# Optimization experiments

Hardware: AMD Instinct MI355X
Metric: run time of the kernel (lower is better)

## Reference

```python
import jax, jax.numpy as jnp
import numpy as np

H = 1024

def setup_inputs() -> dict:
    key = jax.random.key(0)
    ks = jax.random.split(key, 7)
    B, S = 64, 2048
    decoder_hidden = jax.random.normal(ks[0], (B, H), dtype=jnp.float32)
    encoder_outputs = jax.random.normal(ks[1], (B, S, H), dtype=jnp.float32)
    sc = 1.0 / np.sqrt(H)
    W1_w = jax.random.normal(ks[2], (H, H), dtype=jnp.float32) * sc
    W1_b = jax.random.normal(ks[3], (H,), dtype=jnp.float32) * sc
    W2_w = jax.random.normal(ks[4], (H, H), dtype=jnp.float32) * sc
    W2_b = jax.random.normal(ks[5], (H,), dtype=jnp.float32) * sc
    v_w = jax.random.normal(ks[6], (H,), dtype=jnp.float32) * sc
    return {"decoder_hidden": decoder_hidden, "encoder_outputs": encoder_outputs,
            "W1_w": W1_w, "W1_b": W1_b, "W2_w": W2_w, "W2_b": W2_b, "v_w": v_w}

def reference(decoder_hidden, encoder_outputs, W1_w, W1_b, W2_w, W2_b, v_w):
    # enc proj: [B,S,H] @ [H,H] ; dec proj: [B,H] @ [H,H], broadcast over S
    enc_proj = jnp.einsum('bsh,hk->bsk', encoder_outputs, W1_w) + W1_b
    dec_proj = decoder_hidden @ W2_w + W2_b  # [B,H]
    e = jnp.tanh(enc_proj + dec_proj[:, None, :])  # [B,S,H]
    scores = jnp.einsum('bsh,h->bs', e, v_w)  # [B,S]
    attn_weights = jax.nn.softmax(scores, axis=1)
    context = jnp.einsum('bs,bsh->bh', attn_weights, encoder_outputs)
    return (context, attn_weights)
```

## Files before the change

### kernel.cpp

```cpp
#include <hip/hip_runtime.h>
#include <hip/hip_bf16.h>
#include <hip/hip_fp16.h>

#define HDIM 1024
#define BATCH 64
#define SEQ 2048
#define MTOT (BATCH*SEQ)
#define BM 128
#define BN 256
#define BK 64
#define NKT (HDIM/BK)
#define NNT (HDIM/BN)

typedef float f32x4 __attribute__((ext_vector_type(4)));
typedef _Float16 half8 __attribute__((ext_vector_type(8)));
typedef _Float16 half4v __attribute__((ext_vector_type(4)));

static __device__ __forceinline__ void gload_lds16(const void* g, void* l) {
  __builtin_amdgcn_global_load_lds((const __attribute__((address_space(1))) void*)g,
                                   (__attribute__((address_space(3))) void*)l, 16, 0, 0);
}

__global__ void k_w1t(const float* __restrict__ W1, unsigned short* __restrict__ W1T) {
  __shared__ float tile[64][65];
  int h0 = blockIdx.x * 64, k0 = blockIdx.y * 64;
  int t = threadIdx.x;
#pragma unroll
  for (int j = 0; j < 4; ++j) {
    int q = j * 256 + t, r = q >> 4, c = (q & 15) * 4;
    float4 v = *(const float4*)(W1 + (size_t)(h0 + r) * HDIM + k0 + c);
    tile[r][c + 0] = v.x; tile[r][c + 1] = v.y; tile[r][c + 2] = v.z; tile[r][c + 3] = v.w;
  }
  __syncthreads();
#pragma unroll
  for (int j = 0; j < 4; ++j) {
    int q = j * 256 + t, r = q >> 4, c = (q & 15) * 4;
    union { _Float16 h[4]; ushort4 u; } cv;
    cv.h[0] = (_Float16)tile[c + 0][r];
    cv.h[1] = (_Float16)tile[c + 1][r];
    cv.h[2] = (_Float16)tile[c + 2][r];
    cv.h[3] = (_Float16)tile[c + 3][r];
    *(ushort4*)(W1T + (size_t)(k0 + r) * HDIM + h0 + c) = cv.u;
  }
}

__global__ void k_decproj(const float* __restrict__ dh, const float* __restrict__ W2,
                          const float* __restrict__ W2b, float* __restrict__ dp) {
  __shared__ float drow[HDIM];
  int b = blockIdx.x, t = threadIdx.x;
#pragma unroll
  for (int j = 0; j < 4; ++j) drow[j * 256 + t] = dh[(size_t)b * HDIM + j * 256 + t];
  __syncthreads();
  f32x4 acc = {0.f, 0.f, 0.f, 0.f};
#pragma unroll 16
  for (int h = 0; h < HDIM; ++h) {
    float d = drow[h];
    f32x4 w = *(const f32x4*)(W2 + (size_t)h * HDIM + t * 4);
    acc += w * d;
  }
  acc += *(const f32x4*)(W2b + t * 4);
  *(f32x4*)(dp + (size_t)b * HDIM + t * 4) = acc;
}

__global__ __launch_bounds__(512, 4) void k_scores(
    const float* __restrict__ E, const unsigned short* __restrict__ W1T,
    const float* __restrict__ W1b, const float* __restrict__ dp,
    const float* __restrict__ vw, float* __restrict__ spart,
    unsigned short* __restrict__ E16, int we16) {
  __shared__ __align__(16) _Float16 As[BM * BK];
  __shared__ __align__(16) unsigned short Bs[BN * BK];
  float (*scr)[4] = (float(*)[4])As;

  int t = threadIdx.x;
  int bid = blockIdx.x;
  int xcd = bid & 7;
  int q = bid >> 3;
  int mt = (xcd << 7) + (q >> 2);
  int nt = q & 3;
  int m0 = mt * BM, n0 = nt * BN;
  int b = m0 >> 11;

  int lane = t & 63, wid = t >> 6;
  int wr = wid >> 2, wc = wid & 3;
  int l15 = lane & 15, l4 = lane >> 4;

  f32x4 acc[4][4];
#pragma unroll
  for (int i = 0; i < 4; ++i)
#pragma unroll
    for (int j = 0; j < 4; ++j) acc[i][j] = {0.f, 0.f, 0.f, 0.f};

  int ar = t >> 4;
  int ac = (t & 15) * 4;
  int aswz = (((ac >> 3) ^ (ar & 7)) << 4) + ((ac & 7) << 1);
  const float* Ab = E + (size_t)m0 * HDIM;
  unsigned short* e16p = E16 + (size_t)(m0 + nt * 32 + ar) * HDIM + ac;

  float4 areg[4];
#pragma unroll
  for (int j = 0; j < 4; ++j)
    areg[j] = *(const float4*)(Ab + (size_t)(j * 32 + ar) * HDIM + ac);

  for (int kt = 0; kt < NKT; ++kt) {
#pragma unroll
    for (int j = 0; j < 4; ++j) {
      int chunk = wid * 4 + j;
      int row = chunk * 8 + (lane >> 3);
      int u = (lane & 7) ^ (lane >> 3);
      const unsigned short* g = W1T + (size_t)(n0 + row) * HDIM + kt * BK + u * 8;
      gload_lds16(g, (char*)Bs + (size_t)chunk * 1024);
    }

    unsigned long long e16v = 0;
#pragma unroll
    for (int j = 0; j < 4; ++j) {
      union { _Float16 h[4]; unsigned long long u64; } cv;
      cv.h[0] = (_Float16)areg[j].x; cv.h[1] = (_Float16)areg[j].y;
      cv.h[2] = (_Float16)areg[j].z; cv.h[3] = (_Float16)areg[j].w;
      *(unsigned long long*)((char*)As + (j * 32 + ar) * 128 + aswz) = cv.u64;
      if (j == nt) e16v = cv.u64;
    }

    __syncthreads();

    if (we16)
      __builtin_nontemporal_store(e16v, (unsigned long long*)(e16p + kt * BK));

    int ktn = ((kt + 1) & (NKT - 1)) * BK;
#pragma unroll
    for (int j = 0; j < 4; ++j)
      areg[j] = *(const float4*)(Ab + (size_t)(j * 32 + ar) * HDIM + ktn + ac);

    __builtin_amdgcn_s_setprio(1);
#pragma unroll
    for (int ks = 0; ks < 2; ++ks) {
      half8 af[4], bf[4];
#pragma unroll
      for (int mi = 0; mi < 4; ++mi) {
        int row = wr * 64 + mi * 16 + l15;
        af[mi] = *(const half8*)((const char*)As + row * 128 + (((ks * 4 + l4) ^ (row & 7)) << 4));
      }
#pragma unroll
      for (int ni = 0; ni < 4; ++ni) {
        int row = wc * 64 + ni * 16 + l15;
        bf[ni] = *(const half8*)((const char*)Bs + row * 128 + (((ks * 4 + l4) ^ (row & 7)) << 4));
      }
#pragma unroll
      for (int mi = 0; mi < 4; ++mi)
#pragma unroll
        for (int ni = 0; ni < 4; ++ni)
          acc[mi][ni] = __builtin_amdgcn_mfma_f32_16x16x32_f16(af[mi], bf[ni], acc[mi][ni], 0, 0, 0);
    }
    __builtin_amdgcn_s_setprio(0);

    __syncthreads();
  }

  float bias_l[4], v_l[4];
#pragma unroll
  for (int ni = 0; ni < 4; ++ni) {
    int k = n0 + wc * 64 + ni * 16 + l15;
    bias_l[ni] = W1b[k] + dp[(size_t)b * HDIM + k];
    v_l[ni] = vw[k];
  }
#pragma unroll
  for (int mi = 0; mi < 4; ++mi) {
#pragma unroll
    for (int r = 0; r < 4; ++r) {
      float s = 0.f;
#pragma unroll
      for (int ni = 0; ni < 4; ++ni) {
        float x = acc[mi][ni][r] + bias_l[ni];
        float ex = __expf(2.f * x);
        float th = 1.f - 2.f / (ex + 1.f);
        s += th * v_l[ni];
      }
      s += __shfl_xor(s, 1); s += __shfl_xor(s, 2);
      s += __shfl_xor(s, 4); s += __shfl_xor(s, 8);
      if (l15 == 0) scr[wr * 64 + mi * 16 + l4 * 4 + r][wc] = s;
    }
  }
  __syncthreads();
  if (t < BM) {
    f32x4 p = *(const f32x4*)scr[t];
    spart[((size_t)m0 + t) * NNT + nt] = (p[0] + p[1]) + (p[2] + p[3]);
  }
}

__global__ void k_softmax(const float* __restrict__ spart, float* __restrict__ attn) {
  __shared__ float sc[SEQ];
  __shared__ float red[8];
  int b = blockIdx.x, t = threadIdx.x;
  float mx = -1e30f;
#pragma unroll
  for (int j = 0; j < 8; ++j) {
    int s = j * 256 + t;
    f32x4 x = *(const f32x4*)(spart + ((size_t)b * SEQ + s) * NNT);
    float v = (x[0] + x[1]) + (x[2] + x[3]);
    sc[s] = v;
    mx = fmaxf(mx, v);
  }
  for (int m = 1; m < 64; m <<= 1) mx = fmaxf(mx, __shfl_xor(mx, m));
  if ((t & 63) == 0) red[t >> 6] = mx;
  __syncthreads();
  mx = fmaxf(fmaxf(red[0], red[1]), fmaxf(red[2], red[3]));
  float w[8]; float sum = 0.f;
#pragma unroll
  for (int j = 0; j < 8; ++j) {
    float e = __expf(sc[j * 256 + t] - mx);
    w[j] = e; sum += e;
  }
  for (int m = 1; m < 64; m <<= 1) sum += __shfl_xor(sum, m);
  if ((t & 63) == 0) red[4 + (t >> 6)] = sum;
  __syncthreads();
  float inv = 1.f / (red[4] + red[5] + red[6] + red[7]);
#pragma unroll
  for (int j = 0; j < 8; ++j)
    attn[(size_t)b * SEQ + j * 256 + t] = w[j] * inv;
}

__global__ void k_ctx_part(const float* __restrict__ E, const float* __restrict__ attn,
                           float* __restrict__ cpart, int rpc) {
  int b = blockIdx.y, ch = blockIdx.x, nch = gridDim.x;
  int t = threadIdx.x;
  const float* wrow = attn + (size_t)b * SEQ + (size_t)ch * rpc;
  const float* Eb = E + ((size_t)b * SEQ + (size_t)ch * rpc) * HDIM;
  f32x4 acc = {0.f, 0.f, 0.f, 0.f};
#pragma unroll 4
  for (int s = 0; s < rpc; ++s) {
    float w = wrow[s];
    f32x4 e = *(const f32x4*)(Eb + (size_t)s * HDIM + t * 4);
    acc += e * w;
  }
  *(f32x4*)(cpart + ((size_t)b * nch + ch) * HDIM + t * 4) = acc;
}

__global__ void k_ctx_part16(const unsigned short* __restrict__ E16, const float* __restrict__ attn,
                             float* __restrict__ cpart, int rpc) {
  int b = blockIdx.y, ch = blockIdx.x, nch = gridDim.x;
  int t = threadIdx.x;
  const float* wrow = attn + (size_t)b * SEQ + (size_t)ch * rpc;
  const unsigned short* Eb = E16 + ((size_t)b * SEQ + (size_t)ch * rpc) * HDIM;
  f32x4 acc = {0.f, 0.f, 0.f, 0.f};
#pragma unroll 4
  for (int s = 0; s < rpc; ++s) {
    float w = wrow[s];
    half4v e = *(const half4v*)(Eb + (size_t)s * HDIM + t * 4);
    acc[0] += w * (float)e[0];
    acc[1] += w * (float)e[1];
    acc[2] += w * (float)e[2];
    acc[3] += w * (float)e[3];
  }
  *(f32x4*)(cpart + ((size_t)b * nch + ch) * HDIM + t * 4) = acc;
}

__global__ void k_ctx_reduce(const float* __restrict__ cpart, float* __restrict__ ctx, int nch) {
  int idx = blockIdx.x * 256 + threadIdx.x;
  int b = idx >> 10, k = idx & 1023;
  float s = 0.f;
  for (int c = 0; c < nch; ++c) s += cpart[((size_t)(b * nch + c)) * HDIM + k];
  ctx[idx] = s;
}

extern "C" void kernel_launch(void* const* d_in, const int* in_sizes, int n_in,
                              void* d_out, int out_size, void* d_ws, size_t ws_size,
                              hipStream_t stream) {
  const float* dh  = (const float*)d_in[0];
  const float* E   = (const float*)d_in[1];
  const float* W1w = (const float*)d_in[2];
  const float* W1b = (const float*)d_in[3];
  const float* W2w = (const float*)d_in[4];
  const float* W2b = (const float*)d_in[5];
  const float* vw  = (const float*)d_in[6];
  float* out  = (float*)d_out;
  float* ctx  = out;
  float* attn = out + BATCH * HDIM;

  char* ws = (char*)d_ws;
  unsigned short* W1T = (unsigned short*)ws;
  float* dp    = (float*)(ws + (2u << 20));
  float* spart = (float*)(ws + (2u << 20) + (256u << 10));
  float* cpart = (float*)(ws + (6u << 20) + (256u << 10));
  unsigned short* E16 = (unsigned short*)(ws + (14u << 20) + (256u << 10));

  size_t need32  = (6u << 20) + (256u << 10) + (size_t)BATCH * 32 * HDIM * 4;
  size_t needE16 = (14u << 20) + (256u << 10) + (size_t)MTOT * HDIM * 2;
  int nch = (ws_size >= need32) ? 32 : 16;
  int rpc = SEQ / nch;
  int use16 = (ws_size >= needE16) ? 1 : 0;

  k_w1t<<<dim3(16, 16), 256, 0, stream>>>(W1w, W1T);
  k_decproj<<<BATCH, 256, 0, stream>>>(dh, W2w, W2b, dp);
  k_scores<<<(MTOT / BM) * NNT, 512, 0, stream>>>(E, W1T, W1b, dp, vw, spart,
                                                  use16 ? E16 : W1T, use16);
  k_softmax<<<BATCH, 256, 0, stream>>>(spart, attn);
  if (use16)
    k_ctx_part16<<<dim3(nch, BATCH), 256, 0, stream>>>(E16, attn, cpart, rpc);
  else
    k_ctx_part<<<dim3(nch, BATCH), 256, 0, stream>>>(E, attn, cpart, rpc);
  k_ctx_reduce<<<256, 256, 0, stream>>>(cpart, ctx, nch);
}
```

Baseline: 503.1 us.

## Restructure decoder projection to read W2 once and reuse across batch

The decoder projection kernel now assigns each block 16 output columns for all 64 batch rows, instead of one block per batch row. Decoder hidden states are staged transposed in shared memory in chunks of 128. This cuts W2 global traffic from 64 full passes to a single pass. The trade-off is more shared-memory reads and a loop over h chunks with barriers; the column-wise W2 loads are only 64 bytes contiguous per row.

Measured after the change: 540.1 us. 1.07x slower.

```diff
diff --git a/kernel.cpp b/kernel.cpp
--- a/kernel.cpp
+++ b/kernel.cpp
@@ -44,22 +44,42 @@
   }
 }
 
+#define DP_CH 128
 __global__ void k_decproj(const float* __restrict__ dh, const float* __restrict__ W2,
                           const float* __restrict__ W2b, float* __restrict__ dp) {
-  __shared__ float drow[HDIM];
-  int b = blockIdx.x, t = threadIdx.x;
-#pragma unroll
-  for (int j = 0; j < 4; ++j) drow[j * 256 + t] = dh[(size_t)b * HDIM + j * 256 + t];
-  __syncthreads();
-  f32x4 acc = {0.f, 0.f, 0.f, 0.f};
-#pragma unroll 16
-  for (int h = 0; h < HDIM; ++h) {
-    float d = drow[h];
-    f32x4 w = *(const f32x4*)(W2 + (size_t)h * HDIM + t * 4);
-    acc += w * d;
-  }
-  acc += *(const f32x4*)(W2b + t * 4);
-  *(f32x4*)(dp + (size_t)b * HDIM + t * 4) = acc;
+  __shared__ float dhs[DP_CH][65];
+  int kc = blockIdx.x;
+  int t = threadIdx.x;
+  int k = kc * 16 + (t & 15);
+  int bg = t >> 4;
+  float acc[4] = {0.f, 0.f, 0.f, 0.f};
+
+  for (int h0 = 0; h0 < HDIM; h0 += DP_CH) {
+    __syncthreads();
+#pragma unroll
+    for (int it = 0; it < 8; ++it) {
+      int idx = it * 256 + t;
+      int b = idx >> 5;
+      int c4 = (idx & 31) * 4;
+      float4 v = *(const float4*)(dh + (size_t)b * HDIM + h0 + c4);
+      dhs[c4 + 0][b] = v.x;
+      dhs[c4 + 1][b] = v.y;
+      dhs[c4 + 2][b] = v.z;
+      dhs[c4 + 3][b] = v.w;
+    }
+    __syncthreads();
+#pragma unroll 4
+    for (int hh = 0; hh < DP_CH; ++hh) {
+      float w = W2[(size_t)(h0 + hh) * HDIM + k];
+#pragma unroll
+      for (int bi = 0; bi < 4; ++bi)
+        acc[bi] += dhs[hh][bg * 4 + bi] * w;
+    }
+  }
+  float bv = W2b[k];
+#pragma unroll
+  for (int bi = 0; bi < 4; ++bi)
+    dp[(size_t)(bg * 4 + bi) * HDIM + k] = acc[bi] + bv;
 }
 
 __global__ __launch_bounds__(512, 4) void k_scores(
@@ -290,7 +310,7 @@
   int use16 = (ws_size >= needE16) ? 1 : 0;
 
   k_w1t<<<dim3(16, 16), 256, 0, stream>>>(W1w, W1T);
-  k_decproj<<<BATCH, 256, 0, stream>>>(dh, W2w, W2b, dp);
+  k_decproj<<<64, 256, 0, stream>>>(dh, W2w, W2b, dp);
   k_scores<<<(MTOT / BM) * NNT, 512, 0, stream>>>(E, W1T, W1b, dp, vw, spart,
                                                   use16 ? E16 : W1T, use16);
   k_softmax<<<BATCH, 256, 0, stream>>>(spart, attn);
```
